# Optimization experiments

Measured on AMD Instinct MI355X. Metric: run time of the kernel, lower is better.

## Reference

```python
import jax, jax.numpy as jnp
import numpy as np

M_USERS = 100000
N_ITEMS = 50000
NUM_NODES = M_USERS + N_ITEMS
DIM = 64
N_EDGES = 3200000
BATCH = 1024
N_NEGS = 40
REG = 1e-4
NUM_LAYERS = 2


def setup_inputs() -> dict:
    key = jax.random.key(0)
    ks = jax.random.split(key, 14)
    xav = lambda k, shp: jax.random.normal(k, shp, dtype=jnp.float32) * np.float32(np.sqrt(2.0 / (shp[0] + shp[-1])))
    return {
        "E": xav(ks[0], (NUM_NODES, DIM)),
        "E2": xav(ks[1], (NUM_NODES, DIM)),
        "W0": xav(ks[2], (DIM, DIM)),
        "b0": jnp.zeros((DIM,), jnp.float32),
        "W1": xav(ks[3], (DIM, DIM)),
        "b1": jnp.zeros((DIM,), jnp.float32),
        "attn_W": xav(ks[4], (DIM, DIM)),
        "attn_b": jnp.zeros((DIM,), jnp.float32),
        "q_W": xav(ks[5], (1, DIM)),
        "w": jax.random.normal(ks[6], (BATCH,), dtype=jnp.float32),
        "edge_index": jax.random.randint(ks[7], (2, N_EDGES), 0, NUM_NODES, dtype=jnp.int64),
        "u": jax.random.randint(ks[8], (BATCH,), 0, M_USERS, dtype=jnp.int64),
        "v": jax.random.randint(ks[9], (BATCH,), 0, NUM_NODES, dtype=jnp.int64),
        "n": jax.random.randint(ks[10], (BATCH, N_NEGS), 0, NUM_NODES, dtype=jnp.int64),
    }


def _aggregate(E, E2, W0, b0, W1, b1, attn_W, attn_b, q_W, row, col):
    # LightGCN branch: symmetric degree-normalized scatter-add, NUM_LAYERS hops
    deg = jax.ops.segment_sum(jnp.ones_like(col, dtype=E.dtype), col, num_segments=NUM_NODES)
    dinv = jnp.where(deg > 0, jax.lax.rsqrt(jnp.maximum(deg, 1e-12)), 0.0)
    norm = dinv[row] * dinv[col]  # [E]

    def conv(x):
        msg = norm[:, None] * x[row]  # [E, D]
        return jax.ops.segment_sum(msg, col, num_segments=NUM_NODES)

    acc = E
    x = E
    for _ in range(NUM_LAYERS):
        x = conv(x)
        acc = acc + x
    z_p = acc / (NUM_LAYERS + 1)

    # MLP branch (eval mode: dropout disabled)
    h = jax.nn.relu(E2 @ W0.T + b0)
    z_n = jax.nn.relu(h @ W1.T + b1)

    # attention fusion
    w_p = jnp.tanh(z_p @ attn_W.T + attn_b) @ q_W.T  # [NUM_NODES, 1]
    w_n = jnp.tanh(z_n @ attn_W.T + attn_b) @ q_W.T
    alpha = jax.nn.softmax(jnp.concatenate([w_p, w_n], axis=1), axis=1)
    return alpha[:, :1] * z_p + alpha[:, 1:] * z_n


def reference(E, E2, W0, b0, W1, b1, attn_W, attn_b, q_W, w, edge_index, u, v, n):
    row, col = edge_index[0], edge_index[1]
    Z = _aggregate(E, E2, W0, b0, W1, b1, attn_W, attn_b, q_W, row, col)
    u_ = Z[u]            # [B, D]
    v_ = Z[v]            # [B, D]
    n_ = Z[n]            # [B, K, D]
    pos = jnp.sum(u_ * v_, axis=1)                      # [B]
    neg = jnp.einsum('bd,bkd->bk', u_, n_)              # [B, K]
    coef = -0.5 * jnp.sign(w) + 1.5                     # [B]
    sbpr = jax.nn.log_sigmoid(coef[:, None] * pos[:, None] - neg)  # [B, K]
    reg_loss = jnp.sum(u_ ** 2) + jnp.sum(v_ ** 2) + jnp.sum(n_ ** 2)
    return -jnp.sum(sbpr) + REG * reg_loss
```

## Files before the change

kernel.cpp:

```cpp
#include <hip/hip_runtime.h>
#include <hip/hip_fp8.h>
#include <math.h>

#define NUM_NODES 150000
#define DIM 64
#define N_EDGES 3200000
#define BATCH 1024
#define N_NEGS 40
#define REG_COEF 1e-4f

#define BK_BITS 9
#define BK_NODES 512
#define NBK ((NUM_NODES + BK_NODES - 1) >> BK_BITS)
#define TILE 8192
#define NT ((N_EDGES + TILE - 1) / TILE)
#define HSIZE (NBK * NT)
#define SCAN_B 1024
#define NB2 ((HSIZE + SCAN_B - 1) / SCAN_B)
#define NB3 ((NUM_NODES + SCAN_B - 1) / SCAN_B)
#define NLIST (BATCH * (N_NEGS + 2))

typedef _Float16 half2v __attribute__((ext_vector_type(2)));
typedef _Float16 half4v __attribute__((ext_vector_type(4)));

__global__ __launch_bounds__(256) void histo_kernel(const int* __restrict__ col,
                                                    int* __restrict__ hist) {
    __shared__ int h[NBK];
    int t = threadIdx.x;
    for (int i = t; i < NBK; i += 256) h[i] = 0;
    __syncthreads();
    int e0 = blockIdx.x * TILE;
    int e1 = e0 + TILE; if (e1 > N_EDGES) e1 = N_EDGES;
    for (int i = e0 + t; i < e1; i += 256) atomicAdd(&h[col[i] >> BK_BITS], 1);
    __syncthreads();
    for (int i = t; i < NBK; i += 256) hist[i * NT + blockIdx.x] = h[i];
}

__global__ void scan_partial_kernel(const int* __restrict__ src, int* __restrict__ partial, int n) {
    int t = threadIdx.x;
    int g = blockIdx.x * SCAN_B + t;
    int v = (g < n) ? src[g] : 0;
    for (int m = 1; m < 64; m <<= 1) v += __shfl_xor(v, m);
    __shared__ int ws[16];
    if ((t & 63) == 0) ws[t >> 6] = v;
    __syncthreads();
    if (t < 16) {
        int s = ws[t];
        for (int m = 1; m < 16; m <<= 1) s += __shfl_xor(s, m);
        if (t == 0) partial[blockIdx.x] = s;
    }
}

__global__ void scan_base_kernel(int* __restrict__ partial, int nb, int chunks) {
    int l = threadIdx.x;
    int carry = 0;
    for (int c = 0; c < chunks; c++) {
        int idx = c * 64 + l;
        int v = (idx < nb) ? partial[idx] : 0;
        int inc = v;
        for (int m = 1; m < 64; m <<= 1) {
            int t = __shfl_up(inc, m);
            if (l >= m) inc += t;
        }
        int excl = inc - v + carry;
        if (idx < nb) partial[idx] = excl;
        carry += __shfl(inc, 63);
    }
}

__global__ void scan_apply_kernel(int* __restrict__ data, const int* __restrict__ partial, int n) {
    __shared__ int lds[SCAN_B];
    int t = threadIdx.x;
    int g = blockIdx.x * SCAN_B + t;
    int v = (g < n) ? data[g] : 0;
    int val = v;
    lds[t] = val;
    __syncthreads();
    for (int o = 1; o < SCAN_B; o <<= 1) {
        int add = (t >= o) ? lds[t - o] : 0;
        __syncthreads();
        val += add;
        lds[t] = val;
        __syncthreads();
    }
    if (g < n) data[g] = partial[blockIdx.x] + val - v;
}

__global__ void scan_apply2_kernel(const int* __restrict__ src, int* __restrict__ dst,
                                   const int* __restrict__ partial, int n) {
    __shared__ int lds[SCAN_B];
    int t = threadIdx.x;
    int g = blockIdx.x * SCAN_B + t;
    int v = (g < n) ? src[g] : 0;
    int val = v;
    lds[t] = val;
    __syncthreads();
    for (int o = 1; o < SCAN_B; o <<= 1) {
        int add = (t >= o) ? lds[t - o] : 0;
        __syncthreads();
        val += add;
        lds[t] = val;
        __syncthreads();
    }
    if (g < n) dst[g] = partial[blockIdx.x] + val - v;
}

__global__ __launch_bounds__(256) void partition_kernel(const int* __restrict__ row,
                                                        const int* __restrict__ col,
                                                        const int* __restrict__ hist,
                                                        unsigned* __restrict__ staging) {
    __shared__ int base[NBK];
    __shared__ int cnt[NBK];
    int t = threadIdx.x;
    for (int i = t; i < NBK; i += 256) { base[i] = hist[i * NT + blockIdx.x]; cnt[i] = 0; }
    __syncthreads();
    int e0 = blockIdx.x * TILE;
    int e1 = e0 + TILE; if (e1 > N_EDGES) e1 = N_EDGES;
    for (int i = e0 + t; i < e1; i += 256) {
        int c = col[i];
        int b = c >> BK_BITS;
        int r = atomicAdd(&cnt[b], 1);
        staging[base[b] + r] = ((unsigned)(c & (BK_NODES - 1)) << 18) | (unsigned)row[i];
    }
}

__global__ __launch_bounds__(512) void fill3_kernel(const int* __restrict__ hist,
                                                    const unsigned* __restrict__ staging,
                                                    const float* __restrict__ E,
                                                    int* __restrict__ off,
                                                    float* __restrict__ dinv,
                                                    float* __restrict__ sq,
                                                    int* __restrict__ csr_row,
                                                    __hip_fp8x4_e4m3* __restrict__ xnE4) {
    __shared__ int cnt[BK_NODES];
    __shared__ int lds[BK_NODES];
    __shared__ float sdinv[BK_NODES];
    int b = blockIdx.x;
    int t = threadIdx.x;
    int node0 = b << BK_BITS;
    int bstart = hist[b * NT];
    int bend = (b + 1 < NBK) ? hist[(b + 1) * NT] : N_EDGES;
    cnt[t] = 0;
    __syncthreads();
    for (int i = bstart + t; i < bend; i += 512) atomicAdd(&cnt[staging[i] >> 18], 1);
    __syncthreads();
    int v = cnt[t];
    int val = v;
    lds[t] = val;
    __syncthreads();
    for (int o = 1; o < BK_NODES; o <<= 1) {
        int add = (t >= o) ? lds[t - o] : 0;
        __syncthreads();
        val += add;
        lds[t] = val;
        __syncthreads();
    }
    int cursor = bstart + val - v;
    int node = node0 + t;
    float dv = (v > 0) ? rsqrtf((float)v) : 0.f;
    if (node < NUM_NODES) {
        off[node] = cursor;
        dinv[node] = dv;
        sq[node] = sqrtf((float)v);
    }
    sdinv[t] = dv;
    cnt[t] = cursor;
    __syncthreads();
    for (int i = bstart + t; i < bend; i += 512) {
        unsigned s = staging[i];
        int pos = atomicAdd(&cnt[s >> 18], 1);
        csr_row[pos] = (int)(s & 0x3FFFFu);
    }
    int nvalid = NUM_NODES - node0; if (nvalid > BK_NODES) nvalid = BK_NODES;
    int groups = nvalid << 4;
    const float4* E4 = (const float4*)E + ((size_t)node0 << 4);
    __hip_fp8x4_e4m3* out4 = xnE4 + ((size_t)node0 << 4);
    for (int gi = t; gi < groups; gi += 512) {
        float4 e = E4[gi];
        float s = 16.f * sdinv[gi >> 4];
        out4[gi] = __hip_fp8x4_e4m3(make_float4(s * e.x, s * e.y, s * e.z, s * e.w));
    }
    if (b == 0 && t == 0) off[NUM_NODES] = N_EDGES;
}

__global__ void flag_kernel(const int* __restrict__ u, const int* __restrict__ v,
                            const int* __restrict__ n, int* __restrict__ flags) {
    int i = blockIdx.x * blockDim.x + threadIdx.x;
    if (i >= NLIST) return;
    int id;
    if (i < BATCH) id = u[i];
    else if (i < 2 * BATCH) id = v[i - BATCH];
    else id = n[i - 2 * BATCH];
    flags[id] = 1;
}

__global__ void emit_list_kernel(const int* __restrict__ flags, const int* __restrict__ posb,
                                 int* __restrict__ list, int* __restrict__ count) {
    int i = blockIdx.x * blockDim.x + threadIdx.x;
    if (i >= NUM_NODES) return;
    if (flags[i]) list[posb[i]] = i;
    if (i == NUM_NODES - 1) *count = posb[i] + flags[i];
}

__global__ __launch_bounds__(256) void conv1_kernel(const int* __restrict__ off,
                                                    const int* __restrict__ csr_row,
                                                    const float* __restrict__ dinv,
                                                    const __hip_fp8x4_e4m3* __restrict__ xq,
                                                    _Float16* __restrict__ yh) {
    int gid = blockIdx.x * blockDim.x + threadIdx.x;
    int grp = gid >> 4;
    int g = threadIdx.x & 15;
    if (grp >= NUM_NODES) return;
    int start = off[grp];
    int end = off[grp + 1];
    float a0 = 0.f, a1 = 0.f, a2 = 0.f, a3 = 0.f;
    int i = start;
    for (; i + 7 < end; i += 8) {
        int r[8];
#pragma unroll
        for (int k = 0; k < 8; k++) r[k] = csr_row[i + k];
        float4 v[8];
#pragma unroll
        for (int k = 0; k < 8; k++) v[k] = static_cast<float4>(xq[((size_t)r[k] << 4) + g]);
#pragma unroll
        for (int k = 0; k < 8; k++) {
            a0 += v[k].x; a1 += v[k].y; a2 += v[k].z; a3 += v[k].w;
        }
    }
    for (; i < end; ++i) {
        int r = csr_row[i];
        float4 v = static_cast<float4>(xq[((size_t)r << 4) + g]);
        a0 += v.x; a1 += v.y; a2 += v.z; a3 += v.w;
    }
    float dv = dinv[grp];
    float s = dv * dv * (1.f / 16.f);
    union { _Float16 h[4]; short4 s4; } u;
    u.h[0] = (_Float16)(s * a0);
    u.h[1] = (_Float16)(s * a1);
    u.h[2] = (_Float16)(s * a2);
    u.h[3] = (_Float16)(s * a3);
    ((short4*)yh)[((size_t)grp << 4) + g] = u.s4;
}

__global__ __launch_bounds__(256) void conv2_kernel(const int* __restrict__ off,
                                                    const int* __restrict__ csr_row,
                                                    const float* __restrict__ dinv,
                                                    const _Float16* __restrict__ xh,
                                                    float* __restrict__ x2,
                                                    const int* __restrict__ list,
                                                    const int* __restrict__ count) {
    int gid = blockIdx.x * blockDim.x + threadIdx.x;
    int li = gid >> 4;
    int g = threadIdx.x & 15;
    if (li >= *count) return;
    int nd = list[li];
    int start = off[nd];
    int end = off[nd + 1];
    const short4* xh4 = (const short4*)xh;
    float a0 = 0.f, a1 = 0.f, a2 = 0.f, a3 = 0.f;
    int i = start;
    for (; i + 3 < end; i += 4) {
        int r0 = csr_row[i];
        int r1 = csr_row[i + 1];
        int r2 = csr_row[i + 2];
        int r3 = csr_row[i + 3];
        union { short4 s4; _Float16 h[4]; } u0, u1, u2, u3;
        u0.s4 = xh4[((size_t)r0 << 4) + g];
        u1.s4 = xh4[((size_t)r1 << 4) + g];
        u2.s4 = xh4[((size_t)r2 << 4) + g];
        u3.s4 = xh4[((size_t)r3 << 4) + g];
        a0 += (float)u0.h[0] + (float)u1.h[0] + (float)u2.h[0] + (float)u3.h[0];
        a1 += (float)u0.h[1] + (float)u1.h[1] + (float)u2.h[1] + (float)u3.h[1];
        a2 += (float)u0.h[2] + (float)u1.h[2] + (float)u2.h[2] + (float)u3.h[2];
        a3 += (float)u0.h[3] + (float)u1.h[3] + (float)u2.h[3] + (float)u3.h[3];
    }
    for (; i < end; ++i) {
        int r = csr_row[i];
        union { short4 s4; _Float16 h[4]; } u;
        u.s4 = xh4[((size_t)r << 4) + g];
        a0 += (float)u.h[0]; a1 += (float)u.h[1];
        a2 += (float)u.h[2]; a3 += (float)u.h[3];
    }
    float dv = dinv[nd];
    ((float4*)x2)[((size_t)nd << 4) + g] = make_float4(dv * a0, dv * a1, dv * a2, dv * a3);
}

__global__ __launch_bounds__(256, 4) void fuse_kernel(
    const float* __restrict__ E, const float* __restrict__ E2,
    const float* __restrict__ W0, const float* __restrict__ b0,
    const float* __restrict__ W1, const float* __restrict__ b1,
    const float* __restrict__ AW, const float* __restrict__ ab,
    const float* __restrict__ qW,
    const _Float16* __restrict__ xn1, const float* __restrict__ sq,
    const float* x2, float* Z,
    const int* __restrict__ list, const int* __restrict__ count) {
    __shared__ __align__(16) _Float16 W0h[4096];
    __shared__ __align__(16) _Float16 W1h[4096];
    __shared__ __align__(16) _Float16 AWh[4096];
    __shared__ float bb0[64], bb1[64], bab[64], qb[64];
    __shared__ __align__(16) _Float16 xb[4][64];
    __shared__ __align__(16) _Float16 hb[4][64];
    __shared__ __align__(16) _Float16 zpb[4][64];
    __shared__ __align__(16) _Float16 znb[4][64];

    int t = threadIdx.x;
    for (int idx = t; idx < 4096; idx += 256) {
        int j = idx >> 6, k = idx & 63;
        int dst = (k >> 2) * 256 + j * 4 + (k & 3);
        W0h[dst] = (_Float16)W0[idx];
        W1h[dst] = (_Float16)W1[idx];
        AWh[dst] = (_Float16)AW[idx];
    }
    if (t < 64) { bb0[t] = b0[t]; bb1[t] = b1[t]; bab[t] = ab[t]; qb[t] = qW[t]; }
    __syncthreads();

    const int lane = t & 63, w = t >> 6;
    const int cnt = *count;
    const int stride = gridDim.x * 4;
    int li = blockIdx.x * 4 + w;
    if (li >= cnt) return;

    int ndA = list[li];
    size_t bA0 = ((size_t)ndA << 6) + lane;
    float eA = E[bA0], e2A = E2[bA0], x2A = x2[bA0], sqA = sq[ndA];
    _Float16 xnA = xn1[bA0];

    for (; li < cnt; li += stride) {
        int liB = li + stride; liB = (liB < cnt) ? liB : (cnt - 1);
        int ndB = list[liB];
        size_t bB = ((size_t)ndB << 6) + lane;
        float eB = E[bB], e2B = E2[bB], x2B = x2[bB], sqB = sq[ndB];
        _Float16 xnB = xn1[bB];

        size_t base = ((size_t)ndA << 6) + lane;
        float x1v = sqA * (float)xnA;
        float zp = (eA + x1v + x2A) * (1.f / 3.f);
        zpb[w][lane] = (_Float16)zp;
        xb[w][lane] = (_Float16)e2A;
        __builtin_amdgcn_wave_barrier();

        float s0 = bb0[lane], s1 = 0.f;
#pragma unroll
        for (int k4 = 0; k4 < 16; k4++) {
            half4v w4 = *(const half4v*)&W0h[k4 * 256 + lane * 4];
            half4v x4 = *(const half4v*)&xb[w][k4 * 4];
            s0 = __builtin_amdgcn_fdot2((half2v){w4.x, w4.y}, (half2v){x4.x, x4.y}, s0, false);
            s1 = __builtin_amdgcn_fdot2((half2v){w4.z, w4.w}, (half2v){x4.z, x4.w}, s1, false);
        }
        float h = fmaxf(s0 + s1, 0.f);
        hb[w][lane] = (_Float16)h;
        __builtin_amdgcn_wave_barrier();

        s0 = bb1[lane]; s1 = 0.f;
#pragma unroll
        for (int k4 = 0; k4 < 16; k4++) {
            half4v w4 = *(const half4v*)&W1h[k4 * 256 + lane * 4];
            half4v x4 = *(const half4v*)&hb[w][k4 * 4];
            s0 = __builtin_amdgcn_fdot2((half2v){w4.x, w4.y}, (half2v){x4.x, x4.y}, s0, false);
            s1 = __builtin_amdgcn_fdot2((half2v){w4.z, w4.w}, (half2v){x4.z, x4.w}, s1, false);
        }
        float zn = fmaxf(s0 + s1, 0.f);
        znb[w][lane] = (_Float16)zn;
        __builtin_amdgcn_wave_barrier();

        float sp0 = bab[lane], sp1 = 0.f, sn0 = 0.f, sn1 = 0.f;
#pragma unroll
        for (int k4 = 0; k4 < 16; k4++) {
            half4v w4 = *(const half4v*)&AWh[k4 * 256 + lane * 4];
            half4v p4 = *(const half4v*)&zpb[w][k4 * 4];
            half4v n4 = *(const half4v*)&znb[w][k4 * 4];
            sp0 = __builtin_amdgcn_fdot2((half2v){w4.x, w4.y}, (half2v){p4.x, p4.y}, sp0, false);
            sp1 = __builtin_amdgcn_fdot2((half2v){w4.z, w4.w}, (half2v){p4.z, p4.w}, sp1, false);
            sn0 = __builtin_amdgcn_fdot2((half2v){w4.x, w4.y}, (half2v){n4.x, n4.y}, sn0, false);
            sn1 = __builtin_amdgcn_fdot2((half2v){w4.z, w4.w}, (half2v){n4.z, n4.w}, sn1, false);
        }
        float tp = tanhf(sp0 + sp1) * qb[lane];
        float tn = tanhf(bab[lane] + sn0 + sn1) * qb[lane];
        for (int m = 1; m < 64; m <<= 1) {
            tp += __shfl_xor(tp, m);
            tn += __shfl_xor(tn, m);
        }
        float mx = fmaxf(tp, tn);
        float ep = expf(tp - mx), en = expf(tn - mx);
        float inv = 1.f / (ep + en);
        Z[base] = (ep * zp + en * zn) * inv;
        __builtin_amdgcn_wave_barrier();

        ndA = ndB; eA = eB; e2A = e2B; xnA = xnB; x2A = x2B; sqA = sqB;
    }
}

__global__ __launch_bounds__(256) void loss_kernel(const float* __restrict__ Z,
                                                   const float* __restrict__ wv,
                                                   const int* __restrict__ u,
                                                   const int* __restrict__ v,
                                                   const int* __restrict__ n,
                                                   float* __restrict__ out) {
    int wid = (blockIdx.x * blockDim.x + threadIdx.x) >> 6;
    int lane = threadIdx.x & 63;
    if (wid >= BATCH) return;
    float uu = Z[(size_t)u[wid] * DIM + lane];
    float vv = Z[(size_t)v[wid] * DIM + lane];
    float pos = uu * vv;
    for (int m = 1; m < 64; m <<= 1) pos += __shfl_xor(pos, m);
    float reg = uu * uu + vv * vv;
    float wval = wv[wid];
    float sgn = (wval > 0.f ? 1.f : 0.f) - (wval < 0.f ? 1.f : 0.f);
    float coef = -0.5f * sgn + 1.5f;
    float cp = coef * pos;
    float sb = 0.f;
    for (int k = 0; k < N_NEGS; k++) {
        int nid = n[wid * N_NEGS + k];
        float nn = Z[(size_t)nid * DIM + lane];
        float d = uu * nn;
        for (int m = 1; m < 64; m <<= 1) d += __shfl_xor(d, m);
        reg += nn * nn;
        float x = cp - d;
        float ls = (x >= 0.f) ? -log1pf(expf(-x)) : (x - log1pf(expf(x)));
        sb += ls;
    }
    for (int m = 1; m < 64; m <<= 1) reg += __shfl_xor(reg, m);
    if (lane == 0) atomicAdd(out, -sb + REG_COEF * reg);
}

extern "C" void kernel_launch(void* const* d_in, const int* in_sizes, int n_in,
                              void* d_out, int out_size, void* d_ws, size_t ws_size,
                              hipStream_t stream) {
    const float* E  = (const float*)d_in[0];
    const float* E2 = (const float*)d_in[1];
    const float* W0 = (const float*)d_in[2];
    const float* b0 = (const float*)d_in[3];
    const float* W1 = (const float*)d_in[4];
    const float* b1 = (const float*)d_in[5];
    const float* AW = (const float*)d_in[6];
    const float* ab = (const float*)d_in[7];
    const float* qW = (const float*)d_in[8];
    const float* wv = (const float*)d_in[9];
    const int* ei   = (const int*)d_in[10];
    const int* uu   = (const int*)d_in[11];
    const int* vv   = (const int*)d_in[12];
    const int* nn   = (const int*)d_in[13];
    const int* row = ei;
    const int* col = ei + N_EDGES;

    char* ws = (char*)d_ws;
    size_t p = 0;
    auto align_up = [](size_t x) { return (x + 255) & ~(size_t)255; };
    int* off        = (int*)(ws + p); p = align_up(p + (size_t)(NUM_NODES + 1) * 4);
    float* dinv     = (float*)(ws + p); p = align_up(p + (size_t)NUM_NODES * 4);
    float* sq       = (float*)(ws + p); p = align_up(p + (size_t)NUM_NODES * 4);
    int* hist       = (int*)(ws + p); p = align_up(p + (size_t)HSIZE * 4);
    int* partial    = (int*)(ws + p); p = align_up(p + (size_t)NB2 * 4);
    int* csr_row    = (int*)(ws + p); p = align_up(p + (size_t)N_EDGES * 4);
    int* flagi      = (int*)(ws + p); p = align_up(p + (size_t)NUM_NODES * 4);
    int* posb       = (int*)(ws + p); p = align_up(p + (size_t)NUM_NODES * 4);
    int* list       = (int*)(ws + p); p = align_up(p + (size_t)NLIST * 4);
    int* count      = (int*)(ws + p); p = align_up(p + 4);
    __hip_fp8x4_e4m3* xnE4 = (__hip_fp8x4_e4m3*)(ws + p); p = align_up(p + (size_t)NUM_NODES * DIM);
    _Float16* xn1   = (_Float16*)(ws + p); p = align_up(p + (size_t)NUM_NODES * DIM * 2);
    float* x2f      = (float*)(ws + p); p = align_up(p + (size_t)NUM_NODES * DIM * 4);
    float* Z = x2f;
    unsigned* staging = (unsigned*)x2f;

    hipMemsetAsync(d_out, 0, sizeof(float), stream);
    hipMemsetAsync(flagi, 0, (size_t)NUM_NODES * 4, stream);

    histo_kernel<<<NT, 256, 0, stream>>>(col, hist);
    scan_partial_kernel<<<NB2, SCAN_B, 0, stream>>>(hist, partial, HSIZE);
    scan_base_kernel<<<1, 64, 0, stream>>>(partial, NB2, 2);
    scan_apply_kernel<<<NB2, SCAN_B, 0, stream>>>(hist, partial, HSIZE);
    partition_kernel<<<NT, 256, 0, stream>>>(row, col, hist, staging);
    fill3_kernel<<<NBK, 512, 0, stream>>>(hist, staging, E, off, dinv, sq, csr_row, xnE4);

    flag_kernel<<<(NLIST + 255) / 256, 256, 0, stream>>>(uu, vv, nn, flagi);
    scan_partial_kernel<<<NB3, SCAN_B, 0, stream>>>(flagi, partial, NUM_NODES);
    scan_base_kernel<<<1, 64, 0, stream>>>(partial, NB3, 3);
    scan_apply2_kernel<<<NB3, SCAN_B, 0, stream>>>(flagi, posb, partial, NUM_NODES);
    emit_list_kernel<<<(NUM_NODES + 255) / 256, 256, 0, stream>>>(flagi, posb, list, count);

    conv1_kernel<<<(NUM_NODES * 16 + 255) / 256, 256, 0, stream>>>(off, csr_row, dinv, xnE4, xn1);
    conv2_kernel<<<(NLIST * 16 + 255) / 256, 256, 0, stream>>>(off, csr_row, dinv, xn1, x2f, list, count);

    fuse_kernel<<<1280, 256, 0, stream>>>(E, E2, W0, b0, W1, b1, AW, ab, qW,
                                          xn1, sq, x2f, Z, list, count);

    loss_kernel<<<BATCH * 64 / 256, 256, 0, stream>>>(Z, wv, uu, vv, nn, (float*)d_out);
}
```

Measured before the change: 272.4 us.

## Split fused MLP/attention kernel into gather, two MLP, and attention kernels

Replaces the single fused kernel, which ran both MLP layers and the attention step per node with software prefetch, by four kernels. The first gathers z_p and E2 into compact fp16 buffers indexed by list position. Two launches of a shared MLP kernel apply W0 and W1 in place, and an attention kernel combines the results and scatters into Z. This lowers per-kernel LDS use (one weight matrix each) so occupancy should rise, at the cost of extra launches and compact-buffer round trips through memory. The compact buffers reuse the csr_row workspace, which is no longer needed at that point.

Result: slower. 294.8 us (+8.2%).

```diff
diff --git a/kernel.cpp b/kernel.cpp
--- a/kernel.cpp
+++ b/kernel.cpp
@@ -285,97 +285,102 @@
     ((float4*)x2)[((size_t)nd << 4) + g] = make_float4(dv * a0, dv * a1, dv * a2, dv * a3);
 }
 
-__global__ __launch_bounds__(256, 4) void fuse_kernel(
-    const float* __restrict__ E, const float* __restrict__ E2,
-    const float* __restrict__ W0, const float* __restrict__ b0,
-    const float* __restrict__ W1, const float* __restrict__ b1,
-    const float* __restrict__ AW, const float* __restrict__ ab,
-    const float* __restrict__ qW,
-    const _Float16* __restrict__ xn1, const float* __restrict__ sq,
-    const float* x2, float* Z,
-    const int* __restrict__ list, const int* __restrict__ count) {
-    __shared__ __align__(16) _Float16 W0h[4096];
-    __shared__ __align__(16) _Float16 W1h[4096];
-    __shared__ __align__(16) _Float16 AWh[4096];
-    __shared__ float bb0[64], bb1[64], bab[64], qb[64];
-    __shared__ __align__(16) _Float16 xb[4][64];
-    __shared__ __align__(16) _Float16 hb[4][64];
-    __shared__ __align__(16) _Float16 zpb[4][64];
-    __shared__ __align__(16) _Float16 znb[4][64];
-
+__global__ __launch_bounds__(256) void gatherz_kernel(const float* __restrict__ E,
+                                                      const float* __restrict__ E2,
+                                                      const _Float16* __restrict__ xn1,
+                                                      const float* __restrict__ sq,
+                                                      const float* __restrict__ x2,
+                                                      const int* __restrict__ list,
+                                                      const int* __restrict__ count,
+                                                      _Float16* __restrict__ zpc,
+                                                      _Float16* __restrict__ xc) {
+    int gid = blockIdx.x * blockDim.x + threadIdx.x;
+    int li = gid >> 6, lane = gid & 63;
+    if (li >= *count) return;
+    int nd = list[li];
+    size_t b = ((size_t)nd << 6) + lane;
+    float zp = (E[b] + sq[nd] * (float)xn1[b] + x2[b]) * (1.f / 3.f);
+    size_t c = ((size_t)li << 6) + lane;
+    zpc[c] = (_Float16)zp;
+    xc[c] = (_Float16)E2[b];
+}
+
+__global__ __launch_bounds__(256) void mlp_kernel(const float* __restrict__ W,
+                                                  const float* __restrict__ bias,
+                                                  const _Float16* xin,
+                                                  _Float16* xout,
+                                                  const int* __restrict__ count) {
+    __shared__ __align__(16) _Float16 Wh[4096];
+    __shared__ float bb[64];
+    __shared__ __align__(16) _Float16 xs[4][64];
     int t = threadIdx.x;
     for (int idx = t; idx < 4096; idx += 256) {
         int j = idx >> 6, k = idx & 63;
-        int dst = (k >> 2) * 256 + j * 4 + (k & 3);
-        W0h[dst] = (_Float16)W0[idx];
-        W1h[dst] = (_Float16)W1[idx];
-        AWh[dst] = (_Float16)AW[idx];
-    }
-    if (t < 64) { bb0[t] = b0[t]; bb1[t] = b1[t]; bab[t] = ab[t]; qb[t] = qW[t]; }
-    __syncthreads();
-
+        Wh[(k >> 2) * 256 + j * 4 + (k & 3)] = (_Float16)W[idx];
+    }
+    if (t < 64) bb[t] = bias[t];
+    __syncthreads();
     const int lane = t & 63, w = t >> 6;
     const int cnt = *count;
-    const int stride = gridDim.x * 4;
-    int li = blockIdx.x * 4 + w;
-    if (li >= cnt) return;
-
-    int ndA = list[li];
-    size_t bA0 = ((size_t)ndA << 6) + lane;
-    float eA = E[bA0], e2A = E2[bA0], x2A = x2[bA0], sqA = sq[ndA];
-    _Float16 xnA = xn1[bA0];
-
-    for (; li < cnt; li += stride) {
-        int liB = li + stride; liB = (liB < cnt) ? liB : (cnt - 1);
-        int ndB = list[liB];
-        size_t bB = ((size_t)ndB << 6) + lane;
-        float eB = E[bB], e2B = E2[bB], x2B = x2[bB], sqB = sq[ndB];
-        _Float16 xnB = xn1[bB];
-
-        size_t base = ((size_t)ndA << 6) + lane;
-        float x1v = sqA * (float)xnA;
-        float zp = (eA + x1v + x2A) * (1.f / 3.f);
-        zpb[w][lane] = (_Float16)zp;
-        xb[w][lane] = (_Float16)e2A;
+    for (int li = blockIdx.x * 4 + w; li < cnt; li += gridDim.x * 4) {
+        size_t c = ((size_t)li << 6) + lane;
+        xs[w][lane] = xin[c];
         __builtin_amdgcn_wave_barrier();
-
-        float s0 = bb0[lane], s1 = 0.f;
+        float s0 = bb[lane], s1 = 0.f;
 #pragma unroll
         for (int k4 = 0; k4 < 16; k4++) {
-            half4v w4 = *(const half4v*)&W0h[k4 * 256 + lane * 4];
-            half4v x4 = *(const half4v*)&xb[w][k4 * 4];
+            half4v w4 = *(const half4v*)&Wh[k4 * 256 + lane * 4];
+            half4v x4 = *(const half4v*)&xs[w][k4 * 4];
             s0 = __builtin_amdgcn_fdot2((half2v){w4.x, w4.y}, (half2v){x4.x, x4.y}, s0, false);
             s1 = __builtin_amdgcn_fdot2((half2v){w4.z, w4.w}, (half2v){x4.z, x4.w}, s1, false);
         }
-        float h = fmaxf(s0 + s1, 0.f);
-        hb[w][lane] = (_Float16)h;
+        _Float16 r = (_Float16)fmaxf(s0 + s1, 0.f);
         __builtin_amdgcn_wave_barrier();
-
-        s0 = bb1[lane]; s1 = 0.f;
-#pragma unroll
-        for (int k4 = 0; k4 < 16; k4++) {
-            half4v w4 = *(const half4v*)&W1h[k4 * 256 + lane * 4];
-            half4v x4 = *(const half4v*)&hb[w][k4 * 4];
-            s0 = __builtin_amdgcn_fdot2((half2v){w4.x, w4.y}, (half2v){x4.x, x4.y}, s0, false);
-            s1 = __builtin_amdgcn_fdot2((half2v){w4.z, w4.w}, (half2v){x4.z, x4.w}, s1, false);
-        }
-        float zn = fmaxf(s0 + s1, 0.f);
-        znb[w][lane] = (_Float16)zn;
+        xout[c] = r;
         __builtin_amdgcn_wave_barrier();
-
-        float sp0 = bab[lane], sp1 = 0.f, sn0 = 0.f, sn1 = 0.f;
+    }
+}
+
+__global__ __launch_bounds__(256) void attn_kernel(const float* __restrict__ AW,
+                                                   const float* __restrict__ ab,
+                                                   const float* __restrict__ qW,
+                                                   const _Float16* __restrict__ zpc,
+                                                   const _Float16* __restrict__ znc,
+                                                   const int* __restrict__ list,
+                                                   const int* __restrict__ count,
+                                                   float* __restrict__ Z) {
+    __shared__ __align__(16) _Float16 AWh[4096];
+    __shared__ float bab[64], qb[64];
+    __shared__ __align__(16) _Float16 zps[4][64];
+    __shared__ __align__(16) _Float16 zns[4][64];
+    int t = threadIdx.x;
+    for (int idx = t; idx < 4096; idx += 256) {
+        int j = idx >> 6, k = idx & 63;
+        AWh[(k >> 2) * 256 + j * 4 + (k & 3)] = (_Float16)AW[idx];
+    }
+    if (t < 64) { bab[t] = ab[t]; qb[t] = qW[t]; }
+    __syncthreads();
+    const int lane = t & 63, w = t >> 6;
+    const int cnt = *count;
+    for (int li = blockIdx.x * 4 + w; li < cnt; li += gridDim.x * 4) {
+        size_t c = ((size_t)li << 6) + lane;
+        _Float16 zpl = zpc[c], znl = znc[c];
+        zps[w][lane] = zpl;
+        zns[w][lane] = znl;
+        __builtin_amdgcn_wave_barrier();
+        float sp0 = bab[lane], sp1 = 0.f, sn0 = bab[lane], sn1 = 0.f;
 #pragma unroll
         for (int k4 = 0; k4 < 16; k4++) {
             half4v w4 = *(const half4v*)&AWh[k4 * 256 + lane * 4];
-            half4v p4 = *(const half4v*)&zpb[w][k4 * 4];
-            half4v n4 = *(const half4v*)&znb[w][k4 * 4];
+            half4v p4 = *(const half4v*)&zps[w][k4 * 4];
+            half4v n4 = *(const half4v*)&zns[w][k4 * 4];
             sp0 = __builtin_amdgcn_fdot2((half2v){w4.x, w4.y}, (half2v){p4.x, p4.y}, sp0, false);
             sp1 = __builtin_amdgcn_fdot2((half2v){w4.z, w4.w}, (half2v){p4.z, p4.w}, sp1, false);
             sn0 = __builtin_amdgcn_fdot2((half2v){w4.x, w4.y}, (half2v){n4.x, n4.y}, sn0, false);
             sn1 = __builtin_amdgcn_fdot2((half2v){w4.z, w4.w}, (half2v){n4.z, n4.w}, sn1, false);
         }
         float tp = tanhf(sp0 + sp1) * qb[lane];
-        float tn = tanhf(bab[lane] + sn0 + sn1) * qb[lane];
+        float tn = tanhf(sn0 + sn1) * qb[lane];
         for (int m = 1; m < 64; m <<= 1) {
             tp += __shfl_xor(tp, m);
             tn += __shfl_xor(tn, m);
@@ -383,10 +388,9 @@
         float mx = fmaxf(tp, tn);
         float ep = expf(tp - mx), en = expf(tn - mx);
         float inv = 1.f / (ep + en);
-        Z[base] = (ep * zp + en * zn) * inv;
+        int nd = list[li];
+        Z[((size_t)nd << 6) + lane] = (ep * (float)zpl + en * (float)znl) * inv;
         __builtin_amdgcn_wave_barrier();
-
-        ndA = ndB; eA = eB; e2A = e2B; xnA = xnB; x2A = x2B; sqA = sqB;
     }
 }
 
@@ -461,6 +465,8 @@
     float* x2f      = (float*)(ws + p); p = align_up(p + (size_t)NUM_NODES * DIM * 4);
     float* Z = x2f;
     unsigned* staging = (unsigned*)x2f;
+    _Float16* zpc = (_Float16*)csr_row;
+    _Float16* bufA = zpc + (size_t)NLIST * DIM;
 
     hipMemsetAsync(d_out, 0, sizeof(float), stream);
     hipMemsetAsync(flagi, 0, (size_t)NUM_NODES * 4, stream);
@@ -481,8 +487,11 @@
     conv1_kernel<<<(NUM_NODES * 16 + 255) / 256, 256, 0, stream>>>(off, csr_row, dinv, xnE4, xn1);
     conv2_kernel<<<(NLIST * 16 + 255) / 256, 256, 0, stream>>>(off, csr_row, dinv, xn1, x2f, list, count);
 
-    fuse_kernel<<<1280, 256, 0, stream>>>(E, E2, W0, b0, W1, b1, AW, ab, qW,
-                                          xn1, sq, x2f, Z, list, count);
+    gatherz_kernel<<<(NLIST * 64 + 255) / 256, 256, 0, stream>>>(E, E2, xn1, sq, x2f,
+                                                                 list, count, zpc, bufA);
+    mlp_kernel<<<2688, 256, 0, stream>>>(W0, b0, bufA, bufA, count);
+    mlp_kernel<<<2688, 256, 0, stream>>>(W1, b1, bufA, bufA, count);
+    attn_kernel<<<2688, 256, 0, stream>>>(AW, ab, qW, zpc, bufA, list, count, Z);
 
     loss_kernel<<<BATCH * 64 / 256, 256, 0, stream>>>(Z, wv, uu, vv, nn, (float*)d_out);
 }
```
